# Optimization experiments

Hardware: AMD Instinct MI355X
Metric: run time of the kernel (lower is better)

Reference implementation:

```python
import jax, jax.numpy as jnp
import numpy as np

EMB_DIM = 768
N_HEAD = 12
SEQ_LEN = 577  # 24*24 patches + 1 cls token
MAX_RD = 24
GRID = 24
HEAD_DIM = EMB_DIM // N_HEAD
SCALING = HEAD_DIM ** (-0.5)


def _make_dis():
    # 2D grid coordinates per patch; cls token prepended with index 0 (the pad value).
    xs = np.tile(np.arange(GRID), GRID)      # x (column) coordinate of each patch
    ys = np.repeat(np.arange(GRID), GRID)    # y (row) coordinate of each patch

    def rel(p):
        d = p[None, :] - p[:, None]          # pos.unsqueeze(0) - pos.unsqueeze(1)
        d = np.clip(d, -MAX_RD, MAX_RD) + MAX_RD + 1
        return np.pad(d, ((1, 0), (1, 0)))   # cls row/col -> index 0

    return jnp.asarray(rel(xs)), jnp.asarray(rel(ys))  # each (N, N) int32


X_DIS, Y_DIS = _make_dis()


def _pos_emb(x_emb, y_emb):
    # (N, N, HEAD_DIM): concat of x- and y-relative embeddings
    return jnp.concatenate([x_emb[X_DIS], y_emb[Y_DIS]], axis=-1)


def setup_inputs() -> dict:
    key = jax.random.key(0)
    ks = jax.random.split(key, 7)
    s = 0.02
    return {
        "x": jax.random.normal(ks[0], (16, SEQ_LEN, EMB_DIM), dtype=jnp.float32),
        "qkv_w": jax.random.normal(ks[1], (3 * EMB_DIM, EMB_DIM), dtype=jnp.float32) * s,
        "proj_w": jax.random.normal(ks[2], (EMB_DIM, EMB_DIM), dtype=jnp.float32) * s,
        "q_x_emb": jax.random.normal(ks[3], (2 * MAX_RD + 2, HEAD_DIM // 2), dtype=jnp.float32) * s,
        "q_y_emb": jax.random.normal(ks[4], (2 * MAX_RD + 2, HEAD_DIM // 2), dtype=jnp.float32) * s,
        "v_x_emb": jax.random.normal(ks[5], (2 * MAX_RD + 2, HEAD_DIM // 2), dtype=jnp.float32) * s,
        "v_y_emb": jax.random.normal(ks[6], (2 * MAX_RD + 2, HEAD_DIM // 2), dtype=jnp.float32) * s,
    }


def reference(x, qkv_w, proj_w, q_x_emb, q_y_emb, v_x_emb, v_y_emb):
    B, N, C = x.shape
    qkv = (x @ qkv_w.T).reshape(B, N, 3, N_HEAD, HEAD_DIM)
    qkv = jnp.transpose(qkv, (2, 0, 3, 1, 4))  # (3, B, H, N, d)
    q, k, v = qkv[0], qkv[1], qkv[2]

    weight = jnp.einsum("bhnd,bhmd->bhnm", q, k)

    # relative-position bias on the query path:
    # relative_q[b,h,n,m] = sum_d q[b,h,n,d] * q_pos[n,m,d]
    q_pos = _pos_emb(q_x_emb, q_y_emb)                      # (N, N, d)
    weight = weight + jnp.einsum("bhnd,nmd->bhnm", q, q_pos)
    weight = weight * SCALING  # scaling applied after adding relative_q (as in source)

    attn = jax.nn.softmax(weight, axis=-1)                  # (B, H, N, N)

    out = jnp.einsum("bhnm,bhmd->bhnd", attn, v)
    # relative-position contribution on the value path
    v_pos = _pos_emb(v_x_emb, v_y_emb)                      # (N, N, d)
    out = out + jnp.einsum("bhnm,nmd->bhnd", attn, v_pos)

    out = jnp.transpose(out, (0, 2, 1, 3)).reshape(B, N, C)
    return out @ proj_w.T
```

## Files before the change

kernel.cpp:

```cpp
#include <hip/hip_runtime.h>
#include <math.h>

#define SEQ 577
#define NH 12
#define DH 64
#define EMB 768
#define NBATCH 16
#define NC 2
#define BC (NBATCH/NC)
#define MC (BC*SEQ)
#define BHC (BC*NH)
#define VTS 592

typedef float f32x4 __attribute__((ext_vector_type(4)));
typedef short s16x8 __attribute__((ext_vector_type(8)));

__device__ __forceinline__ float bf2f(unsigned short u) {
  union { unsigned int i; float f; } c; c.i = ((unsigned int)u) << 16; return c.f;
}
__device__ __forceinline__ unsigned short f2bf(float f) {
  union { float f; unsigned int i; } c; c.f = f;
  unsigned int r = c.i + 0x7FFFu + ((c.i >> 16) & 1u);
  return (unsigned short)(r >> 16);
}

__device__ __forceinline__ void gl_lds16(const unsigned short* g, unsigned short* l) {
  __builtin_amdgcn_global_load_lds(
      (const __attribute__((address_space(1))) unsigned int*)g,
      (__attribute__((address_space(3))) unsigned int*)l, 16, 0, 0);
}

__global__ __launch_bounds__(256) void cast_kernel(
    const float* __restrict__ s, unsigned short* __restrict__ d, int n4)
{
  int i = blockIdx.x * 256 + threadIdx.x;
  if (i < n4) {
    float4 v = *(const float4*)&s[(size_t)i*4];
    ushort4 o; o.x = f2bf(v.x); o.y = f2bf(v.y); o.z = f2bf(v.z); o.w = f2bf(v.w);
    *(ushort4*)&d[(size_t)i*4] = o;
  }
}

#define TVP 66
__global__ __launch_bounds__(256) void vtrans_kernel(
    const unsigned short* __restrict__ v, unsigned short* __restrict__ vt)
{
  __shared__ __align__(16) unsigned short T[64*TVP];
  const int tid = threadIdx.x;
  const int bh = blockIdx.y;
  const int n0 = blockIdx.x * 64;
  const s16x8 z8 = {0,0,0,0,0,0,0,0};
  {
    int r = tid >> 2, seg = tid & 3;
    int n = n0 + r;
    s16x8 a0 = z8, a1 = z8;
    if (n < SEQ) {
      const unsigned short* src = &v[((size_t)bh*SEQ + n)*DH + seg*16];
      a0 = *(const s16x8*)&src[0];
      a1 = *(const s16x8*)&src[8];
    }
    *(s16x8*)&T[r*TVP + seg*16]     = a0;
    *(s16x8*)&T[r*TVP + seg*16 + 8] = a1;
  }
  __syncthreads();
  {
    int d = tid >> 2, jseg = tid & 3;
    int jb = jseg * 16;
    unsigned short* dst = &vt[((size_t)bh*DH + d)*VTS + n0 + jb];
    if (n0 + jb + 15 < SEQ) {
      s16x8 b0, b1;
#pragma unroll
      for (int s = 0; s < 8; ++s) b0[s] = T[(jb + s)*TVP + d];
#pragma unroll
      for (int s = 0; s < 8; ++s) b1[s] = T[(jb + 8 + s)*TVP + d];
      *(s16x8*)&dst[0] = b0;
      *(s16x8*)&dst[8] = b1;
    } else {
      for (int s = 0; s < 16; ++s) {
        if (n0 + jb + s < SEQ) dst[s] = T[(jb + s)*TVP + d];
      }
    }
  }
}

#define GT 128
__global__ __launch_bounds__(256) void gemm_bf16(
    const unsigned short* __restrict__ A, const unsigned short* __restrict__ Bm,
    unsigned short* __restrict__ Cq, unsigned short* __restrict__ Ck,
    unsigned short* __restrict__ Cv, float* __restrict__ Cf,
    int M, int N, int mode)
{
  __shared__ __align__(16) unsigned short AsF[2][GT*32];
  __shared__ __align__(16) unsigned short BsF[2][GT*32];
  const int tid = threadIdx.x;
  const int wave = tid >> 6;
  const int lane = tid & 63;
  const int wr = wave >> 1, wc = wave & 1;
  const int li = lane & 15, g = lane >> 4;
  const int r0 = blockIdx.y * GT, c0 = blockIdx.x * GT;

  const int row1 = tid >> 2,          seg1 = tid & 3;
  const int row2 = (tid + 256) >> 2,  seg2 = tid & 3;
  const unsigned short* ga1 = &A [(size_t)(r0 + row1)*EMB + seg1*8];
  const unsigned short* ga2 = &A [(size_t)(r0 + row2)*EMB + seg2*8];
  const unsigned short* gb1 = &Bm[(size_t)(c0 + row1)*EMB + seg1*8];
  const unsigned short* gb2 = &Bm[(size_t)(c0 + row2)*EMB + seg2*8];

  f32x4 acc[4][4];
#pragma unroll
  for (int i = 0; i < 4; ++i)
#pragma unroll
    for (int j = 0; j < 4; ++j) { acc[i][j][0]=0.f; acc[i][j][1]=0.f; acc[i][j][2]=0.f; acc[i][j][3]=0.f; }

  gl_lds16(ga1, &AsF[0][wave*512]);
  gl_lds16(ga2, &AsF[0][2048 + wave*512]);
  gl_lds16(gb1, &BsF[0][wave*512]);
  gl_lds16(gb2, &BsF[0][2048 + wave*512]);

  int cur = 0;
  for (int k0 = 0; k0 < EMB; k0 += 32) {
    __syncthreads();
    if (k0 + 32 < EMB) {
      int kn = k0 + 32;
      gl_lds16(ga1 + kn, &AsF[cur^1][wave*512]);
      gl_lds16(ga2 + kn, &AsF[cur^1][2048 + wave*512]);
      gl_lds16(gb1 + kn, &BsF[cur^1][wave*512]);
      gl_lds16(gb2 + kn, &BsF[cur^1][2048 + wave*512]);
    }

    s16x8 af[4], bfv[4];
#pragma unroll
    for (int i = 0; i < 4; ++i) af[i]  = *(const s16x8*)&AsF[cur][(wr*64 + i*16 + li)*32 + g*8];
#pragma unroll
    for (int j = 0; j < 4; ++j) bfv[j] = *(const s16x8*)&BsF[cur][(wc*64 + j*16 + li)*32 + g*8];
#pragma unroll
    for (int i = 0; i < 4; ++i)
#pragma unroll
      for (int j = 0; j < 4; ++j)
        acc[i][j] = __builtin_amdgcn_mfma_f32_16x16x32_bf16(af[i], bfv[j], acc[i][j], 0, 0, 0);
    cur ^= 1;
  }

  if (mode == 1) {
#pragma unroll
    for (int i = 0; i < 4; ++i) {
      int rbase = r0 + wr*64 + i*16 + g*4;
#pragma unroll
      for (int rg = 0; rg < 4; ++rg) {
        int gr = rbase + rg;
        if (gr >= M) continue;
        float* crow = &Cf[(size_t)gr*N + c0 + wc*64 + li];
#pragma unroll
        for (int j = 0; j < 4; ++j) crow[j*16] = acc[i][j][rg];
      }
    }
  } else {
    unsigned short* cb[4]; size_t coff[4];
#pragma unroll
    for (int j = 0; j < 4; ++j) {
      int col = c0 + wc*64 + j*16 + li;
      int t  = col / EMB;
      int ct = col - t*EMB;
      int h  = ct >> 6, dd = ct & 63;
      cb[j]   = (t == 0) ? Cq : (t == 1) ? Ck : Cv;
      coff[j] = (size_t)h*SEQ*DH + dd;
    }
#pragma unroll
    for (int i = 0; i < 4; ++i) {
      int rbase = r0 + wr*64 + i*16 + g*4;
#pragma unroll
      for (int rg = 0; rg < 4; ++rg) {
        int gr = rbase + rg;
        if (gr >= M) continue;
        int brow = gr / SEQ, nrow = gr - brow*SEQ;
        size_t roff = ((size_t)brow*NH)*SEQ*DH + (size_t)nrow*DH;
#pragma unroll
        for (int j = 0; j < 4; ++j)
          cb[j][roff + coff[j]] = f2bf(acc[i][j][rg]);
      }
    }
  }
}

#define TRB 16
#define SW 584

#define FOR_KT(X) X(0) X(1) X(2) X(3) X(4) X(5) X(6) X(7) X(8) X(9)

__global__ __launch_bounds__(256) void attn_kernel(
    const unsigned short* __restrict__ qg, const unsigned short* __restrict__ kg,
    const unsigned short* __restrict__ vtg,
    const float* __restrict__ qxe, const float* __restrict__ qye,
    const float* __restrict__ vxe, const float* __restrict__ vye,
    unsigned short* __restrict__ og)
{
  __shared__ __align__(16) unsigned short Ps[TRB][SW];
  __shared__ __align__(16) unsigned char  TBCS[3392];
  __shared__ __align__(16) float red[TRB][4];
  __shared__ __align__(16) unsigned short VXL[50*32];
  __shared__ __align__(16) unsigned short VYL[50*32];

  const int tid  = threadIdx.x;
  const int wave = tid >> 6, lane = tid & 63;
  const int li = lane & 15, gg = lane >> 4;
  const int bh = blockIdx.y;
  const int r0 = blockIdx.x * TRB;
  const size_t qkbase = (size_t)bh * SEQ * DH;
  const size_t vtbase = (size_t)bh * DH * VTS;
  const s16x8 z8 = {0,0,0,0,0,0,0,0};

  for (int t4 = tid; t4 < 400; t4 += 256) {
    float4 a = ((const float4*)vxe)[t4];
    float4 b = ((const float4*)vye)[t4];
    ushort4 oa; oa.x=f2bf(a.x); oa.y=f2bf(a.y); oa.z=f2bf(a.z); oa.w=f2bf(a.w);
    ushort4 ob; ob.x=f2bf(b.x); ob.y=f2bf(b.y); ob.z=f2bf(b.z); ob.w=f2bf(b.w);
    ((ushort4*)VXL)[t4] = oa;
    ((ushort4*)VYL)[t4] = ob;
  }

  s16x8 qf0, qf1;
  {
    int n = r0 + li;
    qf0 = (n < SEQ) ? *(const s16x8*)&qg[qkbase + (size_t)n*DH + gg*8] : z8;
    qf1 = (n < SEQ) ? *(const s16x8*)&qg[qkbase + (size_t)n*DH + 32 + gg*8] : z8;
  }

  const unsigned short* kwv = &kg[qkbase + (size_t)(wave*16 + li)*DH];
  s16x8 kp0 = *(const s16x8*)&kwv[gg*8];
  s16x8 kp1 = *(const s16x8*)&kwv[32 + gg*8];

  unsigned short* TB = (unsigned short*)TBCS;
  {
    int bin = wave*16 + li;
    s16x8 bx = z8, by = z8;
    if (bin < 50) {
      float4 x0 = *(const float4*)&qxe[bin*32 + gg*8];
      float4 x1 = *(const float4*)&qxe[bin*32 + gg*8 + 4];
      float4 y0 = *(const float4*)&qye[bin*32 + gg*8];
      float4 y1 = *(const float4*)&qye[bin*32 + gg*8 + 4];
      bx[0]=f2bf(x0.x); bx[1]=f2bf(x0.y); bx[2]=f2bf(x0.z); bx[3]=f2bf(x0.w);
      bx[4]=f2bf(x1.x); bx[5]=f2bf(x1.y); bx[6]=f2bf(x1.z); bx[7]=f2bf(x1.w);
      by[0]=f2bf(y0.x); by[1]=f2bf(y0.y); by[2]=f2bf(y0.z); by[3]=f2bf(y0.w);
      by[4]=f2bf(y1.x); by[5]=f2bf(y1.y); by[6]=f2bf(y1.z); by[7]=f2bf(y1.w);
    }
    f32x4 ax0={0.f,0.f,0.f,0.f}, ay0={0.f,0.f,0.f,0.f};
    ax0 = __builtin_amdgcn_mfma_f32_16x16x32_bf16(qf0, bx, ax0, 0,0,0);
    ay0 = __builtin_amdgcn_mfma_f32_16x16x32_bf16(qf1, by, ay0, 0,0,0);
    if (bin < 50) {
#pragma unroll
      for (int rg = 0; rg < 4; ++rg) {
        TB[(gg*4+rg)*104      + bin] = f2bf(ax0[rg]);
        TB[(gg*4+rg)*104 + 52 + bin] = f2bf(ay0[rg]);
      }
    }
  }

  int xn[4], yn[4];
#pragma unroll
  for (int rg = 0; rg < 4; ++rg) {
    int n = r0 + gg*4 + rg;
    if (n > 0 && n <= SEQ) { xn[rg] = (n-1) % 24; yn[rg] = (n-1) / 24; }
    else { xn[rg] = 0; yn[rg] = 0; }
  }
  __syncthreads();

  f32x4 LpA = {0.f,0.f,0.f,0.f};

#define KTSTEP(KT) do {                                                       \
    const int m0_ = (KT)*64;                                                  \
    s16x8 kc0_ = kp0, kc1_ = kp1;                                             \
    if ((KT) < 9) {                                                           \
      kp0 = *(const s16x8*)&kwv[(size_t)(m0_ + 64)*DH + gg*8];                \
      kp1 = *(const s16x8*)&kwv[(size_t)(m0_ + 64)*DH + 32 + gg*8];           \
    }                                                                         \
    f32x4 a0_ = {0.f,0.f,0.f,0.f};                                            \
    a0_ = __builtin_amdgcn_mfma_f32_16x16x32_bf16(qf0, kc0_, a0_, 0,0,0);     \
    a0_ = __builtin_amdgcn_mfma_f32_16x16x32_bf16(qf1, kc1_, a0_, 0,0,0);     \
    int m_ = m0_ + wave*16 + li;                                              \
    int xm_ = 0, ym_ = 0;                                                     \
    bool mv_ = (m_ > 0 && m_ < SEQ);                                          \
    if (mv_) { xm_ = (m_-1) % 24; ym_ = (m_-1) / 24; }                        \
    _Pragma("unroll")                                                         \
    for (int rg = 0; rg < 4; ++rg) {                                          \
      int nloc_ = gg*4 + rg; int n_ = r0 + nloc_;                             \
      float s_ = a0_[rg]; int xi_ = 0, yi_ = 0;                               \
      if (mv_ && n_ > 0) { xi_ = xm_ - xn[rg] + 25; yi_ = ym_ - yn[rg] + 25; }\
      s_ = (s_ + bf2f(TB[nloc_*104 + xi_]) + bf2f(TB[nloc_*104 + 52 + yi_])) * 0.125f; \
      float p_ = (m_ < SEQ) ? __expf(s_) : 0.f;                               \
      LpA[rg] += p_;                                                          \
      if (m_ < SW) Ps[nloc_][m_] = f2bf(p_);                                  \
    }                                                                         \
  } while (0);
  FOR_KT(KTSTEP)
#undef KTSTEP

  const unsigned short* vwv = &vtg[vtbase + (size_t)(wave*16 + li)*VTS];
  s16x8 vp0 = *(const s16x8*)&vwv[gg*8];
  s16x8 vp1 = *(const s16x8*)&vwv[32 + gg*8];

#pragma unroll
  for (int rg = 0; rg < 4; ++rg) {
    float s = LpA[rg];
    s += __shfl_xor(s, 1); s += __shfl_xor(s, 2);
    s += __shfl_xor(s, 4); s += __shfl_xor(s, 8);
    if (li == 0) red[gg*4 + rg][wave] = s;
  }
  __syncthreads();
  float* CS = (float*)TBCS;
  if (wave == 0 && li == 0) {
#pragma unroll
    for (int rg = 0; rg < 4; ++rg) {
      int nloc = gg*4 + rg;
      float4 r4 = *(float4*)&red[nloc][0];
      CS[nloc*49 + 48] = r4.x + r4.y + r4.z + r4.w;
    }
  }
  {
    int r = tid >> 4, kb = tid & 15;
#pragma unroll
    for (int kk = 0; kk < 3; ++kk) {
      int k = kb + kk*16;
      float s = 0.f;
      if (k < 24) {
#pragma unroll
        for (int c2 = 0; c2 < 24; ++c2) s += bf2f(Ps[r][1 + c2*24 + k]);
      } else {
        int rw = k - 24;
#pragma unroll
        for (int c2 = 0; c2 < 24; ++c2) s += bf2f(Ps[r][1 + rw*24 + c2]);
      }
      CS[r*49 + k] = s;
    }
  }
  __syncthreads();

  f32x4 oa0 = {0.f,0.f,0.f,0.f};
  s16x8 ap0 = *(const s16x8*)&Ps[li][gg*8];
  s16x8 ap1 = *(const s16x8*)&Ps[li][32 + gg*8];
#pragma unroll
  for (int vt = 0; vt < 10; ++vt) {
    s16x8 vc0 = vp0, vc1 = vp1;
    s16x8 ac0 = ap0, ac1 = ap1;
    if (vt < 9) {
      int mn = (vt + 1)*64;
      vp0 = *(const s16x8*)&vwv[mn + gg*8];
      vp1 = *(const s16x8*)&vwv[mn + 32 + gg*8];
      if (vt < 8) {
        ap0 = *(const s16x8*)&Ps[li][mn + gg*8];
        ap1 = *(const s16x8*)&Ps[li][mn + 32 + gg*8];
      } else {
        ap0 = (gg == 0) ? *(const s16x8*)&Ps[li][576] : z8;
        ap1 = z8;
      }
    }
    oa0 = __builtin_amdgcn_mfma_f32_16x16x32_bf16(ac0, vc0, oa0, 0,0,0);
    oa0 = __builtin_amdgcn_mfma_f32_16x16x32_bf16(ac1, vc1, oa0, 0,0,0);
  }

  {
    int d = wave*16 + li;
    const unsigned short* tabL = (d < 32) ? VXL : VYL;
    int dd = d & 31;
    bool useX = (d < 32);
    int bI = bh / NH, hI = bh - bI*NH;
#pragma unroll
    for (int rg = 0; rg < 4; ++rg) {
      int nloc = gg*4 + rg;
      int n = r0 + nloc;
      if (n >= SEQ) continue;
      float Lr = CS[nloc*49 + 48];
      float bias;
      if (n == 0) {
        bias = Lr * bf2f(tabL[dd]);
      } else {
        int cn = useX ? ((n-1) % 24) : ((n-1) / 24);
        const unsigned short* trow = &tabL[(25 - cn)*32 + dd];
        const float* csrow = &CS[nloc*49 + (useX ? 0 : 24)];
        float b0 = bf2f(Ps[nloc][0]) * bf2f(tabL[dd]);
        float b1 = 0.f, b2 = 0.f, b3 = 0.f;
#pragma unroll
        for (int c = 0; c < 24; c += 4) {
          b0 = fmaf(csrow[c    ], bf2f(trow[(c    )*32]), b0);
          b1 = fmaf(csrow[c + 1], bf2f(trow[(c + 1)*32]), b1);
          b2 = fmaf(csrow[c + 2], bf2f(trow[(c + 2)*32]), b2);
          b3 = fmaf(csrow[c + 3], bf2f(trow[(c + 3)*32]), b3);
        }
        bias = (b0 + b1) + (b2 + b3);
      }
      float o = (oa0[rg] + bias) / Lr;
      og[(((size_t)bI*SEQ + n)*NH + hI)*DH + d] = f2bf(o);
    }
  }
}

extern "C" void kernel_launch(void* const* d_in, const int* in_sizes, int n_in,
                              void* d_out, int out_size, void* d_ws, size_t ws_size,
                              hipStream_t stream)
{
  const float* x     = (const float*)d_in[0];
  const float* qkvw  = (const float*)d_in[1];
  const float* projw = (const float*)d_in[2];
  const float* qxe   = (const float*)d_in[3];
  const float* qye   = (const float*)d_in[4];
  const float* vxe   = (const float*)d_in[5];
  const float* vye   = (const float*)d_in[6];
  float* out = (float*)d_out;

  const size_t SLc = (size_t)BHC * SEQ * DH;
  const size_t VTL = (size_t)BHC * DH * VTS;
  unsigned short* qws   = (unsigned short*)d_ws;
  unsigned short* kws   = qws + SLc;
  unsigned short* vtws  = kws + SLc;
  unsigned short* ows   = vtws + VTL;
  unsigned short* xbf   = ows + SLc;
  unsigned short* wqkv  = xbf + SLc;
  unsigned short* wproj = wqkv + (size_t)3*EMB*EMB;
  unsigned short* vtmp  = wproj + (size_t)EMB*EMB;

  cast_kernel<<<(3*EMB*EMB/4 + 255)/256, 256, 0, stream>>>(qkvw, wqkv, 3*EMB*EMB/4);
  cast_kernel<<<(EMB*EMB/4 + 255)/256, 256, 0, stream>>>(projw, wproj, EMB*EMB/4);

  dim3 g1(3*EMB/GT, (MC + GT - 1)/GT);
  dim3 gt(10, BHC);
  dim3 g2((SEQ + TRB - 1)/TRB, BHC);
  dim3 g3(EMB/GT, (MC + GT - 1)/GT);

  for (int c = 0; c < NC; ++c) {
    const float* xc = x   + (size_t)c * MC * EMB;
    float*       oc = out + (size_t)c * MC * EMB;
    cast_kernel<<<(MC*EMB/4 + 255)/256, 256, 0, stream>>>(xc, xbf, MC*EMB/4);
    gemm_bf16<<<g1, 256, 0, stream>>>(xbf, wqkv, qws, kws, vtmp, nullptr, MC, 3*EMB, 0);
    vtrans_kernel<<<gt, 256, 0, stream>>>(vtmp, vtws);
    attn_kernel<<<g2, 256, 0, stream>>>(qws, kws, vtws, qxe, qye, vxe, vye, ows);
    gemm_bf16<<<g3, 256, 0, stream>>>(ows, wproj, nullptr, nullptr, nullptr, oc, MC, EMB, 1);
  }
}
```

Measured before the change: 347.0 us.

## Batch output projection across both chunks with a 64-row-tile GEMM kernel

Attention outputs for both batch chunks now go into a doubled workspace, and a single projection GEMM runs over all rows after the loop instead of one per chunk. A new GEMM kernel with 64x128 tiles writes fp32 output directly, which gives more blocks to fill the GPU and removes one launch plus the tail of each per-chunk GEMM. The cost is extra workspace and a smaller tile with less reuse per block. Rows past M are still loaded from A, because the loads have no row guard.

```diff
diff --git a/kernel.cpp b/kernel.cpp
--- a/kernel.cpp
+++ b/kernel.cpp
@@ -178,6 +178,71 @@
         for (int j = 0; j < 4; ++j)
           cb[j][roff + coff[j]] = f2bf(acc[i][j][rg]);
       }
+    }
+  }
+}
+
+__global__ __launch_bounds__(256) void gemm64_kernel(
+    const unsigned short* __restrict__ A, const unsigned short* __restrict__ Bm,
+    float* __restrict__ Cf, int M, int N)
+{
+  __shared__ __align__(16) unsigned short As[2][64*32];
+  __shared__ __align__(16) unsigned short Bs[2][128*32];
+  const int tid = threadIdx.x;
+  const int wave = tid >> 6;
+  const int lane = tid & 63;
+  const int li = lane & 15, g = lane >> 4;
+  const int r0 = blockIdx.y * 64, c0 = blockIdx.x * GT;
+
+  const int rowA = tid >> 2, seg = tid & 3;
+  const int rowB2 = (tid + 256) >> 2;
+  const unsigned short* ga  = &A [(size_t)(r0 + rowA)*EMB + seg*8];
+  const unsigned short* gb1 = &Bm[(size_t)(c0 + rowA)*EMB + seg*8];
+  const unsigned short* gb2 = &Bm[(size_t)(c0 + rowB2)*EMB + seg*8];
+
+  f32x4 acc[4][2];
+#pragma unroll
+  for (int i = 0; i < 4; ++i)
+#pragma unroll
+    for (int j = 0; j < 2; ++j) { acc[i][j][0]=0.f; acc[i][j][1]=0.f; acc[i][j][2]=0.f; acc[i][j][3]=0.f; }
+
+  gl_lds16(ga,  &As[0][wave*512]);
+  gl_lds16(gb1, &Bs[0][wave*512]);
+  gl_lds16(gb2, &Bs[0][2048 + wave*512]);
+
+  int cur = 0;
+  for (int k0 = 0; k0 < EMB; k0 += 32) {
+    __syncthreads();
+    if (k0 + 32 < EMB) {
+      int kn = k0 + 32;
+      gl_lds16(ga + kn,  &As[cur^1][wave*512]);
+      gl_lds16(gb1 + kn, &Bs[cur^1][wave*512]);
+      gl_lds16(gb2 + kn, &Bs[cur^1][2048 + wave*512]);
+    }
+
+    s16x8 af[4], bfv[2];
+#pragma unroll
+    for (int i = 0; i < 4; ++i) af[i]  = *(const s16x8*)&As[cur][(i*16 + li)*32 + g*8];
+#pragma unroll
+    for (int j = 0; j < 2; ++j) bfv[j] = *(const s16x8*)&Bs[cur][(wave*32 + j*16 + li)*32 + g*8];
+#pragma unroll
+    for (int i = 0; i < 4; ++i)
+#pragma unroll
+      for (int j = 0; j < 2; ++j)
+        acc[i][j] = __builtin_amdgcn_mfma_f32_16x16x32_bf16(af[i], bfv[j], acc[i][j], 0, 0, 0);
+    cur ^= 1;
+  }
+
+#pragma unroll
+  for (int i = 0; i < 4; ++i) {
+    int rbase = r0 + i*16 + g*4;
+#pragma unroll
+    for (int rg = 0; rg < 4; ++rg) {
+      int gr = rbase + rg;
+      if (gr >= M) continue;
+      float* crow = &Cf[(size_t)gr*N + c0 + wave*32 + li];
+#pragma unroll
+      for (int j = 0; j < 2; ++j) crow[j*16] = acc[i][j][rg];
     }
   }
 }
@@ -412,7 +477,7 @@
   unsigned short* kws   = qws + SLc;
   unsigned short* vtws  = kws + SLc;
   unsigned short* ows   = vtws + VTL;
-  unsigned short* xbf   = ows + SLc;
+  unsigned short* xbf   = ows + 2*SLc;
   unsigned short* wqkv  = xbf + SLc;
   unsigned short* wproj = wqkv + (size_t)3*EMB*EMB;
   unsigned short* vtmp  = wproj + (size_t)EMB*EMB;
@@ -423,15 +488,15 @@
   dim3 g1(3*EMB/GT, (MC + GT - 1)/GT);
   dim3 gt(10, BHC);
   dim3 g2((SEQ + TRB - 1)/TRB, BHC);
-  dim3 g3(EMB/GT, (MC + GT - 1)/GT);
+  dim3 g3(EMB/GT, (2*MC + 63)/64);
 
   for (int c = 0; c < NC; ++c) {
-    const float* xc = x   + (size_t)c * MC * EMB;
-    float*       oc = out + (size_t)c * MC * EMB;
+    const float* xc = x + (size_t)c * MC * EMB;
     cast_kernel<<<(MC*EMB/4 + 255)/256, 256, 0, stream>>>(xc, xbf, MC*EMB/4);
     gemm_bf16<<<g1, 256, 0, stream>>>(xbf, wqkv, qws, kws, vtmp, nullptr, MC, 3*EMB, 0);
     vtrans_kernel<<<gt, 256, 0, stream>>>(vtmp, vtws);
-    attn_kernel<<<g2, 256, 0, stream>>>(qws, kws, vtws, qxe, qye, vxe, vye, ows);
-    gemm_bf16<<<g3, 256, 0, stream>>>(ows, wproj, nullptr, nullptr, nullptr, oc, MC, EMB, 1);
-  }
-}
+    attn_kernel<<<g2, 256, 0, stream>>>(qws, kws, vtws, qxe, qye, vxe, vye,
+                                        ows + (size_t)c * SLc);
+  }
+  gemm64_kernel<<<g3, 256, 0, stream>>>(ows, wproj, out, 2*MC, EMB);
+}
```

Result: faster. 332.2 us (-4.3%).
